# Optimization experiments

Measured on AMD Instinct MI355X. Metric: run time of the kernel, lower is better.

## Reference

```python
import jax, jax.numpy as jnp
import numpy as np

SYNCNET_T = 5
EMB_D = 512


def _l2norm(x, eps=1e-12):
    return x / jnp.maximum(jnp.linalg.norm(x, axis=-1, keepdims=True), eps)


def setup_inputs() -> dict:
    key = jax.random.key(0)
    k = jax.random.split(key, 6)
    b = 256
    a_1 = jax.random.normal(k[0], (b, 1, 80, 16), dtype=jnp.float32)
    a_2 = jax.random.normal(k[1], (b, 1, 80, 16), dtype=jnp.float32)
    v_1 = jax.random.normal(k[2], (b, 3, SYNCNET_T, 96, 96), dtype=jnp.float32)
    v_2 = jax.random.normal(k[3], (b, 3, SYNCNET_T, 96, 96), dtype=jnp.float32)
    da = 1 * 80 * 16
    dv = 3 * SYNCNET_T * 48 * 96
    W_a = jax.random.normal(k[4], (da, EMB_D), dtype=jnp.float32) / np.float32(np.sqrt(da))
    W_v = jax.random.normal(k[5], (dv, EMB_D), dtype=jnp.float32) / np.float32(np.sqrt(dv))
    return {"a_1": a_1, "v_1": v_1, "a_2": a_2, "v_2": v_2, "W_a": W_a, "W_v": W_v}


def reference(a_1, v_1, a_2, v_2, W_a, W_v):
    b = a_1.shape[0]
    audio = jnp.concatenate([a_1, a_2], axis=0)      # (2b,1,80,16)
    visual = jnp.concatenate([v_1, v_2], axis=0)     # (2b,3,T,96,96)
    visual = visual[:, :, :, visual.shape[3] // 2:]  # lower half -> (2b,3,T,48,96)
    # torch.cat([visual[:,:,i] for i in range(T)], dim=1) -> channel order (T,3)
    n2 = visual.shape[0]
    visual = jnp.moveaxis(visual, 2, 1).reshape(n2, 3 * SYNCNET_T, 48, 96)
    # syncnet (modeled): flatten -> linear -> L2 normalize, 512-d embeddings
    a = _l2norm(audio.reshape(n2, -1) @ W_a)  # (2b,d)
    v = _l2norm(visual.reshape(n2, -1) @ W_v)  # (2b,d)
    a1, a2 = a[:b], a[b:]
    v1, v2 = v[:b], v[b:]
    dot = lambda x, y: jnp.sum(x * y, axis=-1)
    # numerator: product of {a1,a2}x{v1,v2} + combos within audio and within visual
    numerator = (jnp.exp(dot(a1, v1)) + jnp.exp(dot(a1, v2))
                 + jnp.exp(dot(a2, v1)) + jnp.exp(dot(a2, v2))
                 + jnp.exp(dot(a1, a2)) + jnp.exp(dot(v1, v2)))  # (b,)
    # denominator: product of {a1,a2} with ALL visual embeddings v (2b)
    denominator = (jnp.exp(a1 @ v.T) + jnp.exp(a2 @ v.T)).sum(axis=1)  # (b,)
    loss = -jnp.mean(jnp.log(numerator / denominator))
    return loss
```

## Files before the change

kernel.cpp:

```cpp
#include <hip/hip_runtime.h>

typedef __attribute__((ext_vector_type(8))) short bf16x8;
typedef __attribute__((ext_vector_type(4))) float f32x4;

__device__ __forceinline__ unsigned int pk2(float a, float b) {
    unsigned int r;
    asm("v_cvt_pk_bf16_f32 %0, %1, %2" : "=v"(r) : "v"(a), "v"(b));
    return r;
}

__device__ __forceinline__ void gll16(void* lds, const void* g) {
    __builtin_amdgcn_global_load_lds(
        (__attribute__((address_space(1))) void*)(uintptr_t)g,
        (__attribute__((address_space(3))) void*)(uint32_t)(uintptr_t)lds,
        16, 0, 0);
}

__global__ __launch_bounds__(256) void conv_fused(
    const float* __restrict__ v_1, const float* __restrict__ v_2,
    const float* __restrict__ a_1, const float* __restrict__ a_2,
    const float* __restrict__ W_v, const float* __restrict__ W_a,
    unsigned short* __restrict__ Av, unsigned short* __restrict__ Wt,
    unsigned short* __restrict__ Aa, unsigned short* __restrict__ Wat,
    int doAv)
{
    __shared__ float T[64][65];
    const int tid = threadIdx.x;
    const int b = blockIdx.x;

    if (b < 8800) {
        const float* src; unsigned short* dst; int K, kt, nt;
        if (b < 8640) { src = W_v; dst = Wt;  K = 69120; kt = b >> 3; nt = b & 7; }
        else          { src = W_a; dst = Wat; K = 1280;  kt = (b - 8640) >> 3; nt = (b - 8640) & 7; }
        const int k0 = kt * 64, n0 = nt * 64;
        #pragma unroll
        for (int i = 0; i < 4; ++i) {
            const int kr = i * 16 + (tid >> 4);
            const int c4 = tid & 15;
            const float4 f = *(const float4*)(src + (size_t)(k0 + kr) * 512 + n0 + c4 * 4);
            T[c4 * 4 + 0][kr] = f.x; T[c4 * 4 + 1][kr] = f.y;
            T[c4 * 4 + 2][kr] = f.z; T[c4 * 4 + 3][kr] = f.w;
        }
        __syncthreads();
        #pragma unroll
        for (int j = 0; j < 2; ++j) {
            const int id = j * 256 + tid;
            const int nl = id >> 3, u = id & 7;
            float v[8];
            #pragma unroll
            for (int kk = 0; kk < 8; ++kk) v[kk] = T[nl][u * 8 + kk];
            uint4 o;
            o.x = pk2(v[0], v[1]); o.y = pk2(v[2], v[3]);
            o.z = pk2(v[4], v[5]); o.w = pk2(v[6], v[7]);
            *(uint4*)(dst + (size_t)(n0 + nl) * K + k0 + u * 8) = o;
        }
    } else if (b < 16480) {
        if (!doAv) return;
        const int bb = b - 8800;
        const int r = bb / 15, p = bb - r * 15;
        const float* srcb = (r < 256) ? (v_1 + (size_t)r * 138240)
                                      : (v_2 + (size_t)(r - 256) * 138240);
        const int c = p % 3, t9 = p / 3;
        const float* src = srcb + c * 46080 + t9 * 9216 + 4608;
        unsigned short* dst = Av + (size_t)r * 69120 + p * 4608;
        #pragma unroll
        for (int it = 0; it < 5; ++it) {
            const int u = it * 256 + tid;
            if (u < 1152) {
                const float4 f = *(const float4*)(src + u * 4);
                uint2 o; o.x = pk2(f.x, f.y); o.y = pk2(f.z, f.w);
                *(uint2*)(dst + u * 4) = o;
            }
        }
    } else {
        const int idx4 = (b - 16480) * 256 + tid;
        const int row = idx4 / 320;
        const int col4 = idx4 - row * 320;
        const float* src = (row < 256) ? (a_1 + (size_t)row * 1280)
                                       : (a_2 + (size_t)(row - 256) * 1280);
        const float4 f = *(const float4*)(src + col4 * 4);
        uint2 o; o.x = pk2(f.x, f.y); o.y = pk2(f.z, f.w);
        *(uint2*)(Aa + (size_t)idx4 * 4) = o;
    }
}

template<int AMODE>
__global__ __launch_bounds__(256, 3) void gemm_kernel(
    const unsigned short* __restrict__ Abf,
    const float* __restrict__ s1, const float* __restrict__ s2,
    const unsigned short* __restrict__ Bt,
    float* __restrict__ part, int K, int ksteps)
{
    __shared__ uint4 As[1024];
    __shared__ uint4 Bs[1024];

    const int tid = threadIdx.x;
    const int blk = blockIdx.x;
    const int nwg = gridDim.x;
    const int cpx = nwg >> 3;
    const int lin = (blk & 7) * cpx + (blk >> 3);
    const int z  = lin >> 4;
    const int mn = lin & 15;
    const int m0 = (mn >> 2) * 128;
    const int n0 = (mn & 3) * 128;
    const int k0 = z * ksteps * 64;
    part += (size_t)z * 262144;

    const int wid = tid >> 6, lane = tid & 63;
    const int l15 = lane & 15, lk = lane >> 4;
    const int wm = (wid >> 1) * 64, wn = (wid & 1) * 64;

    int ua[2][4], ub[2][4];
    #pragma unroll
    for (int kh = 0; kh < 2; ++kh) {
        #pragma unroll
        for (int mi = 0; mi < 4; ++mi) {
            const int row = wm + mi * 16 + l15;
            ua[kh][mi] = row * 8 + ((kh * 4 + lk) ^ (row & 7));
        }
        #pragma unroll
        for (int ni = 0; ni < 4; ++ni) {
            const int nn = wn + ni * 16 + l15;
            ub[kh][ni] = nn * 8 + ((kh * 4 + lk) ^ (nn & 7));
        }
    }

    const unsigned short* bsrc[4];
    const unsigned short* asrc[4];
    #pragma unroll
    for (int i = 0; i < 4; ++i) {
        const int u = i * 256 + tid;
        const int rw = u >> 3, c = u & 7;
        bsrc[i] = Bt + (size_t)(n0 + rw) * K + k0 + ((c ^ (rw & 7)) * 8);
        if (AMODE == 0)
            asrc[i] = Abf + (size_t)(m0 + rw) * K + k0 + ((c ^ (rw & 7)) * 8);
    }
    const int a_row = tid >> 1;
    const float* abase = nullptr;
    if (AMODE == 1) {
        const int grow = m0 + a_row;
        abase = (grow < 256) ? (s1 + (size_t)grow * 138240)
                             : (s2 + (size_t)(grow - 256) * 138240);
    }

    f32x4 acc[4][4];
    #pragma unroll
    for (int mi = 0; mi < 4; ++mi)
        #pragma unroll
        for (int ni = 0; ni < 4; ++ni) acc[mi][ni] = f32x4{0.f, 0.f, 0.f, 0.f};

    int kc = k0;
    for (int ks = 0; ks < ksteps; ++ks) {
        #pragma unroll
        for (int i = 0; i < 4; ++i)
            gll16(Bs + i * 256 + wid * 64, bsrc[i]);
        if (AMODE == 0) {
            #pragma unroll
            for (int i = 0; i < 4; ++i)
                gll16(As + i * 256 + wid * 64, asrc[i]);
        } else {
            #pragma unroll
            for (int x4 = 0; x4 < 4; ++x4) {
                const int x = (tid & 1) * 4 + x4;
                const int kg = kc + x * 8;
                const int p = kg / 4608;
                const int j = kg - p * 4608;
                const int c3 = p % 3, t9 = p / 3;
                const float* ap = abase + c3 * 46080 + t9 * 9216 + 4608 + j;
                const float4 f0 = *(const float4*)ap;
                const float4 f1 = *(const float4*)(ap + 4);
                uint4 pa;
                pa.x = pk2(f0.x, f0.y); pa.y = pk2(f0.z, f0.w);
                pa.z = pk2(f1.x, f1.y); pa.w = pk2(f1.z, f1.w);
                As[a_row * 8 + (x ^ (a_row & 7))] = pa;
            }
        }
        __syncthreads();

        #pragma unroll
        for (int kh = 0; kh < 2; ++kh) {
            bf16x8 af[4], bfr[4];
            #pragma unroll
            for (int mi = 0; mi < 4; ++mi) af[mi] = __builtin_bit_cast(bf16x8, As[ua[kh][mi]]);
            #pragma unroll
            for (int ni = 0; ni < 4; ++ni) bfr[ni] = __builtin_bit_cast(bf16x8, Bs[ub[kh][ni]]);
            #pragma unroll
            for (int mi = 0; mi < 4; ++mi)
                #pragma unroll
                for (int ni = 0; ni < 4; ++ni)
                    acc[mi][ni] = __builtin_amdgcn_mfma_f32_16x16x32_bf16(af[mi], bfr[ni], acc[mi][ni], 0, 0, 0);
        }
        __syncthreads();

        kc += 64;
        #pragma unroll
        for (int i = 0; i < 4; ++i) bsrc[i] += 64;
        if (AMODE == 0) {
            #pragma unroll
            for (int i = 0; i < 4; ++i) asrc[i] += 64;
        }
    }

    #pragma unroll
    for (int mi = 0; mi < 4; ++mi)
        #pragma unroll
        for (int ni = 0; ni < 4; ++ni) {
            const int col = n0 + wn + ni * 16 + l15;
            #pragma unroll
            for (int r = 0; r < 4; ++r) {
                const int row = m0 + wm + mi * 16 + lk * 4 + r;
                part[(size_t)row * 512 + col] = acc[mi][ni][r];
            }
        }
}

__global__ __launch_bounds__(256) void norm_kernel(
    const float* __restrict__ partA, const float* __restrict__ partV,
    float* __restrict__ Aout, float* __restrict__ Vout, int nzV)
{
    const int row = blockIdx.x;
    const int tid = threadIdx.x;
    const bool isV = row >= 512;
    const int r = isV ? (row - 512) : row;
    const int c0 = tid, c1 = tid + 256;

    float v0 = 0.f, v1 = 0.f;
    if (isV) {
        for (int zz = 0; zz < nzV; ++zz) {
            const float* p = partV + (size_t)zz * 262144 + (size_t)r * 512;
            v0 += p[c0]; v1 += p[c1];
        }
    } else {
        #pragma unroll
        for (int zz = 0; zz < 2; ++zz) {
            const float* p = partA + (size_t)zz * 262144 + (size_t)r * 512;
            v0 += p[c0]; v1 += p[c1];
        }
    }

    float ss = v0 * v0 + v1 * v1;
    #pragma unroll
    for (int off = 32; off > 0; off >>= 1) ss += __shfl_down(ss, off);
    __shared__ float sbuf[4];
    if ((tid & 63) == 0) sbuf[tid >> 6] = ss;
    __syncthreads();
    const float total = sbuf[0] + sbuf[1] + sbuf[2] + sbuf[3];
    const float inv = 1.f / fmaxf(sqrtf(total), 1e-12f);

    float* outp = (isV ? Vout : Aout) + (size_t)r * 512;
    outp[c0] = v0 * inv;
    outp[c1] = v1 * inv;
}

__global__ __launch_bounds__(256) void sim_kernel(
    const float* __restrict__ A, const float* __restrict__ V,
    float* __restrict__ den, float* __restrict__ num)
{
    __shared__ uint4 As[2][256];
    __shared__ uint4 Bs[2][256];

    const int tid = threadIdx.x;
    const int m0 = (blockIdx.x >> 3) * 64;
    const int n0 = (blockIdx.x & 7) * 64;
    const int nsteps = 16;

    const int a_row = tid >> 2, a_kb = tid & 3;
    const int b_col = tid & 63, b_kb = tid >> 6;
    const int a_u = (a_kb * 64 + a_row) ^ (a_kb << 1);
    const int b_u = (b_kb * 64 + b_col) ^ (b_kb << 1);

    const float* abase = A + (size_t)(m0 + a_row) * 512;
    const float* bptr  = V + (size_t)(n0 + b_col) * 512 + b_kb * 8;
    int aoff = a_kb * 8;

    const int lane = tid & 63, wid = tid >> 6;
    const int wrow = (wid >> 1) * 32, wcol = (wid & 1) * 32;
    const int l15 = lane & 15, lk = lane >> 4;

    int ra[2], rb[2];
    #pragma unroll
    for (int m = 0; m < 2; ++m) ra[m] = (lk * 64 + wrow + m * 16 + l15) ^ (lk << 1);
    #pragma unroll
    for (int n = 0; n < 2; ++n) rb[n] = (lk * 64 + wcol + n * 16 + l15) ^ (lk << 1);

    f32x4 acc[2][2];
    #pragma unroll
    for (int m = 0; m < 2; ++m)
        #pragma unroll
        for (int n = 0; n < 2; ++n) acc[m][n] = f32x4{0.f, 0.f, 0.f, 0.f};

    float4 A0 = *(const float4*)(abase + aoff);
    float4 A1 = *(const float4*)(abase + aoff + 4);
    float4 B0 = *(const float4*)bptr;
    float4 B1 = *(const float4*)(bptr + 4);

    for (int ks = 0; ks < nsteps; ++ks) {
        const int cur = ks & 1;
        const bool more = (ks + 1 < nsteps);
        float4 A0n, A1n, B0n, B1n;
        if (more) {
            aoff += 32; bptr += 32;
            A0n = *(const float4*)(abase + aoff);
            A1n = *(const float4*)(abase + aoff + 4);
            B0n = *(const float4*)bptr;
            B1n = *(const float4*)(bptr + 4);
        }
        uint4 pa;
        pa.x = pk2(A0.x, A0.y); pa.y = pk2(A0.z, A0.w);
        pa.z = pk2(A1.x, A1.y); pa.w = pk2(A1.z, A1.w);
        As[cur][a_u] = pa;
        uint4 pb;
        pb.x = pk2(B0.x, B0.y); pb.y = pk2(B0.z, B0.w);
        pb.z = pk2(B1.x, B1.y); pb.w = pk2(B1.z, B1.w);
        Bs[cur][b_u] = pb;
        __syncthreads();

        bf16x8 af[2], bfr[2];
        #pragma unroll
        for (int m = 0; m < 2; ++m) af[m] = __builtin_bit_cast(bf16x8, As[cur][ra[m]]);
        #pragma unroll
        for (int n = 0; n < 2; ++n) bfr[n] = __builtin_bit_cast(bf16x8, Bs[cur][rb[n]]);
        #pragma unroll
        for (int m = 0; m < 2; ++m)
            #pragma unroll
            for (int n = 0; n < 2; ++n)
                acc[m][n] = __builtin_amdgcn_mfma_f32_16x16x32_bf16(af[m], bfr[n], acc[m][n], 0, 0, 0);

        if (more) { A0 = A0n; A1 = A1n; B0 = B0n; B1 = B1n; }
    }

    #pragma unroll
    for (int m = 0; m < 2; ++m) {
        float rs[4] = {0.f, 0.f, 0.f, 0.f};
        #pragma unroll
        for (int n = 0; n < 2; ++n) {
            const int col = n0 + wcol + n * 16 + l15;
            #pragma unroll
            for (int r = 0; r < 4; ++r) {
                const int row = m0 + wrow + m * 16 + lk * 4 + r;
                const float e = __expf(acc[m][n][r]);
                rs[r] += e;
                if (((row - col) & 255) == 0) atomicAdd(num + (row & 255), e);
            }
        }
        #pragma unroll
        for (int r = 0; r < 4; ++r) {
            float v = rs[r];
            v += __shfl_xor(v, 1);
            v += __shfl_xor(v, 2);
            v += __shfl_xor(v, 4);
            v += __shfl_xor(v, 8);
            if (l15 == 0) {
                const int row = m0 + wrow + m * 16 + lk * 4 + r;
                atomicAdd(den + (row & 255), v);
            }
        }
    }
}

__global__ __launch_bounds__(512) void zero_kernel(float* __restrict__ p) {
    p[threadIdx.x] = 0.f;
}

__global__ __launch_bounds__(256) void dots_kernel(
    const float* __restrict__ A, const float* __restrict__ V,
    float* __restrict__ num)
{
    const int b = blockIdx.x;
    const int i = b & 255;
    const float* X = (b < 256) ? A : V;
    const float* x = X + (size_t)i * 512;
    const float* y = X + (size_t)(i + 256) * 512;
    const int tid = threadIdx.x;
    float d = x[tid] * y[tid] + x[tid + 256] * y[tid + 256];
    #pragma unroll
    for (int off = 32; off > 0; off >>= 1) d += __shfl_down(d, off);
    __shared__ float sbuf[4];
    if ((tid & 63) == 0) sbuf[tid >> 6] = d;
    __syncthreads();
    if (tid == 0) atomicAdd(num + i, __expf(sbuf[0] + sbuf[1] + sbuf[2] + sbuf[3]));
}

__global__ __launch_bounds__(256) void final_kernel(
    const float* __restrict__ den, const float* __restrict__ num,
    float* __restrict__ out)
{
    const int tid = threadIdx.x;
    float v = logf(den[tid]) - logf(num[tid]);
    #pragma unroll
    for (int off = 32; off > 0; off >>= 1) v += __shfl_down(v, off);
    __shared__ float sbuf[4];
    if ((tid & 63) == 0) sbuf[tid >> 6] = v;
    __syncthreads();
    if (tid == 0) out[0] = (sbuf[0] + sbuf[1] + sbuf[2] + sbuf[3]) * (1.f / 256.f);
}

extern "C" void kernel_launch(void* const* d_in, const int* in_sizes, int n_in,
                              void* d_out, int out_size, void* d_ws, size_t ws_size,
                              hipStream_t stream)
{
    (void)in_sizes; (void)n_in; (void)out_size;
    const float* a_1 = (const float*)d_in[0];
    const float* v_1 = (const float*)d_in[1];
    const float* a_2 = (const float*)d_in[2];
    const float* v_2 = (const float*)d_in[3];
    const float* W_a = (const float*)d_in[4];
    const float* W_v = (const float*)d_in[5];
    float* out = (float*)d_out;

    const size_t F_BASE = 512  + 2 * 262144  + 2 * 262144
                        + 2 * 327680  + 17694720 ;
    auto bytes_for = [&](int kv, bool av) {
        return (F_BASE + (size_t)kv * 262144 + (av ? 17694720u : 0u)) * 4;
    };
    int KV; bool AV;
    if      (ws_size >= bytes_for(45, true))  { KV = 45; AV = true;  }
    else if (ws_size >= bytes_for(45, false)) { KV = 45; AV = false; }
    else if (ws_size >= bytes_for(15, false)) { KV = 15; AV = false; }
    else                                      { KV = 8;  AV = false; }
    const int kstepsV = 1080 / KV;

    float* cur = (float*)d_ws;
    float* den   = cur; cur += 256;
    float* num   = cur; cur += 256;
    float* Anorm = cur; cur += 262144;
    float* Vnorm = cur; cur += 262144;
    float* partA = cur; cur += 2 * 262144;
    unsigned short* Aa  = (unsigned short*)cur; cur += 327680;
    unsigned short* Wat = (unsigned short*)cur; cur += 327680;
    float* partV = cur; cur += (size_t)KV * 262144;
    unsigned short* Wt = (unsigned short*)cur; cur += 17694720;
    unsigned short* Av = (unsigned short*)cur;

    zero_kernel<<<1, 512, 0, stream>>>(den);

    conv_fused<<<17120, 256, 0, stream>>>(v_1, v_2, a_1, a_2, W_v, W_a,
                                          Av, Wt, Aa, Wat, AV ? 1 : 0);

    if (AV)
        gemm_kernel<0><<<16 * KV, 256, 0, stream>>>(Av, nullptr, nullptr, Wt,
                                                    partV, 69120, kstepsV);
    else
        gemm_kernel<1><<<16 * KV, 256, 0, stream>>>(nullptr, v_1, v_2, Wt,
                                                    partV, 69120, kstepsV);

    gemm_kernel<0><<<32, 256, 0, stream>>>(Aa, nullptr, nullptr, Wat,
                                           partA, 1280, 10);

    norm_kernel<<<1024, 256, 0, stream>>>(partA, partV, Anorm, Vnorm, KV);
    sim_kernel<<<64, 256, 0, stream>>>(Anorm, Vnorm, den, num);
    dots_kernel<<<512, 256, 0, stream>>>(Anorm, Vnorm, num);
    final_kernel<<<1, 256, 0, stream>>>(den, num, out);
}
```

Before: 199.8 us.

## Drop bf16 activation pre-conversion; convert activations inside GEMM and simplify weight transpose

Removes the separate pass that converted the cropped visual and audio activations to bf16 in workspace. Both GEMMs now load fp32 activations directly and pack them to bf16 while staging into LDS, so activations are no longer written out and read back. The weight transpose becomes a simpler kernel: each thread reads one column with strided loads and writes contiguous bf16 runs, with no LDS tile. The workspace split-K fallback levels also change. The risk is that in-GEMM conversion adds VALU work and fp32 global load traffic to the main loop, and the strided column reads in the transpose may coalesce less well.

```diff
diff --git a/kernel.cpp b/kernel.cpp
--- a/kernel.cpp
+++ b/kernel.cpp
@@ -2,6 +2,8 @@
 
 typedef __attribute__((ext_vector_type(8))) short bf16x8;
 typedef __attribute__((ext_vector_type(4))) float f32x4;
+
+#define KSA 2
 
 __device__ __forceinline__ unsigned int pk2(float a, float b) {
     unsigned int r;
@@ -16,77 +18,35 @@
         16, 0, 0);
 }
 
-__global__ __launch_bounds__(256) void conv_fused(
-    const float* __restrict__ v_1, const float* __restrict__ v_2,
-    const float* __restrict__ a_1, const float* __restrict__ a_2,
-    const float* __restrict__ W_v, const float* __restrict__ W_a,
-    unsigned short* __restrict__ Av, unsigned short* __restrict__ Wt,
-    unsigned short* __restrict__ Aa, unsigned short* __restrict__ Wat,
-    int doAv)
-{
-    __shared__ float T[64][65];
-    const int tid = threadIdx.x;
-    const int b = blockIdx.x;
-
-    if (b < 8800) {
-        const float* src; unsigned short* dst; int K, kt, nt;
-        if (b < 8640) { src = W_v; dst = Wt;  K = 69120; kt = b >> 3; nt = b & 7; }
-        else          { src = W_a; dst = Wat; K = 1280;  kt = (b - 8640) >> 3; nt = (b - 8640) & 7; }
-        const int k0 = kt * 64, n0 = nt * 64;
-        #pragma unroll
-        for (int i = 0; i < 4; ++i) {
-            const int kr = i * 16 + (tid >> 4);
-            const int c4 = tid & 15;
-            const float4 f = *(const float4*)(src + (size_t)(k0 + kr) * 512 + n0 + c4 * 4);
-            T[c4 * 4 + 0][kr] = f.x; T[c4 * 4 + 1][kr] = f.y;
-            T[c4 * 4 + 2][kr] = f.z; T[c4 * 4 + 3][kr] = f.w;
-        }
-        __syncthreads();
-        #pragma unroll
-        for (int j = 0; j < 2; ++j) {
-            const int id = j * 256 + tid;
-            const int nl = id >> 3, u = id & 7;
-            float v[8];
-            #pragma unroll
-            for (int kk = 0; kk < 8; ++kk) v[kk] = T[nl][u * 8 + kk];
-            uint4 o;
-            o.x = pk2(v[0], v[1]); o.y = pk2(v[2], v[3]);
-            o.z = pk2(v[4], v[5]); o.w = pk2(v[6], v[7]);
-            *(uint4*)(dst + (size_t)(n0 + nl) * K + k0 + u * 8) = o;
-        }
-    } else if (b < 16480) {
-        if (!doAv) return;
-        const int bb = b - 8800;
-        const int r = bb / 15, p = bb - r * 15;
-        const float* srcb = (r < 256) ? (v_1 + (size_t)r * 138240)
-                                      : (v_2 + (size_t)(r - 256) * 138240);
-        const int c = p % 3, t9 = p / 3;
-        const float* src = srcb + c * 46080 + t9 * 9216 + 4608;
-        unsigned short* dst = Av + (size_t)r * 69120 + p * 4608;
-        #pragma unroll
-        for (int it = 0; it < 5; ++it) {
-            const int u = it * 256 + tid;
-            if (u < 1152) {
-                const float4 f = *(const float4*)(src + u * 4);
-                uint2 o; o.x = pk2(f.x, f.y); o.y = pk2(f.z, f.w);
-                *(uint2*)(dst + u * 4) = o;
-            }
-        }
-    } else {
-        const int idx4 = (b - 16480) * 256 + tid;
-        const int row = idx4 / 320;
-        const int col4 = idx4 - row * 320;
-        const float* src = (row < 256) ? (a_1 + (size_t)row * 1280)
-                                       : (a_2 + (size_t)(row - 256) * 1280);
-        const float4 f = *(const float4*)(src + col4 * 4);
-        uint2 o; o.x = pk2(f.x, f.y); o.y = pk2(f.z, f.w);
-        *(uint2*)(Aa + (size_t)idx4 * 4) = o;
-    }
-}
-
-template<int AMODE>
+__global__ __launch_bounds__(256) void wtrans(
+    const float* __restrict__ Wv, const float* __restrict__ Wa,
+    unsigned short* __restrict__ Wt, unsigned short* __restrict__ Wat)
+{
+    const int b = blockIdx.x, tid = threadIdx.x;
+    const float* src; unsigned short* dst; int K, kbase, n;
+    if (b < 1080) { src = Wv; dst = Wt;  K = 69120; kbase = (b >> 1) * 128; n = (b & 1) * 256 + tid; }
+    else { const int bb = b - 1080;
+           src = Wa; dst = Wat; K = 1280;  kbase = (bb >> 1) * 128; n = (bb & 1) * 256 + tid; }
+
+    const float* sp = src + n;
+    unsigned short* dp = dst + (size_t)n * K + kbase;
+
+    for (int kk = 0; kk < 128; kk += 16) {
+        float v[16];
+        #pragma unroll
+        for (int i = 0; i < 16; ++i) v[i] = sp[(size_t)(kbase + kk + i) * 512];
+        uint4 o0, o1;
+        o0.x = pk2(v[0], v[1]);  o0.y = pk2(v[2], v[3]);
+        o0.z = pk2(v[4], v[5]);  o0.w = pk2(v[6], v[7]);
+        o1.x = pk2(v[8], v[9]);  o1.y = pk2(v[10], v[11]);
+        o1.z = pk2(v[12], v[13]); o1.w = pk2(v[14], v[15]);
+        *(uint4*)(dp + kk) = o0;
+        *(uint4*)(dp + kk + 8) = o1;
+    }
+}
+
+template<int CROP>
 __global__ __launch_bounds__(256, 3) void gemm_kernel(
-    const unsigned short* __restrict__ Abf,
     const float* __restrict__ s1, const float* __restrict__ s2,
     const unsigned short* __restrict__ Bt,
     float* __restrict__ part, int K, int ksteps)
@@ -96,8 +56,7 @@
 
     const int tid = threadIdx.x;
     const int blk = blockIdx.x;
-    const int nwg = gridDim.x;
-    const int cpx = nwg >> 3;
+    const int cpx = gridDim.x >> 3;
     const int lin = (blk & 7) * cpx + (blk >> 3);
     const int z  = lin >> 4;
     const int mn = lin & 15;
@@ -126,22 +85,18 @@
     }
 
     const unsigned short* bsrc[4];
-    const unsigned short* asrc[4];
     #pragma unroll
     for (int i = 0; i < 4; ++i) {
         const int u = i * 256 + tid;
         const int rw = u >> 3, c = u & 7;
         bsrc[i] = Bt + (size_t)(n0 + rw) * K + k0 + ((c ^ (rw & 7)) * 8);
-        if (AMODE == 0)
-            asrc[i] = Abf + (size_t)(m0 + rw) * K + k0 + ((c ^ (rw & 7)) * 8);
-    }
+    }
+
     const int a_row = tid >> 1;
-    const float* abase = nullptr;
-    if (AMODE == 1) {
-        const int grow = m0 + a_row;
-        abase = (grow < 256) ? (s1 + (size_t)grow * 138240)
-                             : (s2 + (size_t)(grow - 256) * 138240);
-    }
+    const int grow = m0 + a_row;
+    const int ROWSTR = CROP ? 138240 : 1280;
+    const float* abase = (grow < 256) ? s1 + (size_t)grow * ROWSTR
+                                      : s2 + (size_t)(grow - 256) * ROWSTR;
 
     f32x4 acc[4][4];
     #pragma unroll
@@ -154,26 +109,26 @@
         #pragma unroll
         for (int i = 0; i < 4; ++i)
             gll16(Bs + i * 256 + wid * 64, bsrc[i]);
-        if (AMODE == 0) {
-            #pragma unroll
-            for (int i = 0; i < 4; ++i)
-                gll16(As + i * 256 + wid * 64, asrc[i]);
+
+        int aoffu;
+        if (CROP) {
+            const int p = kc / 4608;
+            const int j = kc - p * 4608;
+            const int c3 = p % 3, t9 = p / 3;
+            aoffu = c3 * 46080 + t9 * 9216 + 4608 + j;
         } else {
-            #pragma unroll
-            for (int x4 = 0; x4 < 4; ++x4) {
-                const int x = (tid & 1) * 4 + x4;
-                const int kg = kc + x * 8;
-                const int p = kg / 4608;
-                const int j = kg - p * 4608;
-                const int c3 = p % 3, t9 = p / 3;
-                const float* ap = abase + c3 * 46080 + t9 * 9216 + 4608 + j;
-                const float4 f0 = *(const float4*)ap;
-                const float4 f1 = *(const float4*)(ap + 4);
-                uint4 pa;
-                pa.x = pk2(f0.x, f0.y); pa.y = pk2(f0.z, f0.w);
-                pa.z = pk2(f1.x, f1.y); pa.w = pk2(f1.z, f1.w);
-                As[a_row * 8 + (x ^ (a_row & 7))] = pa;
-            }
+            aoffu = kc;
+        }
+        #pragma unroll
+        for (int x4 = 0; x4 < 4; ++x4) {
+            const int x = (tid & 1) * 4 + x4;
+            const float* ap = abase + aoffu + x * 8;
+            const float4 f0 = *(const float4*)ap;
+            const float4 f1 = *(const float4*)(ap + 4);
+            uint4 pa;
+            pa.x = pk2(f0.x, f0.y); pa.y = pk2(f0.z, f0.w);
+            pa.z = pk2(f1.x, f1.y); pa.w = pk2(f1.z, f1.w);
+            As[a_row * 8 + (x ^ (a_row & 7))] = pa;
         }
         __syncthreads();
 
@@ -195,10 +150,6 @@
         kc += 64;
         #pragma unroll
         for (int i = 0; i < 4; ++i) bsrc[i] += 64;
-        if (AMODE == 0) {
-            #pragma unroll
-            for (int i = 0; i < 4; ++i) asrc[i] += 64;
-        }
     }
 
     #pragma unroll
@@ -232,7 +183,7 @@
         }
     } else {
         #pragma unroll
-        for (int zz = 0; zz < 2; ++zz) {
+        for (int zz = 0; zz < KSA; ++zz) {
             const float* p = partA + (size_t)zz * 262144 + (size_t)r * 512;
             v0 += p[c0]; v1 += p[c1];
         }
@@ -408,46 +359,34 @@
     const float* W_v = (const float*)d_in[5];
     float* out = (float*)d_out;
 
-    const size_t F_BASE = 512  + 2 * 262144  + 2 * 262144
-                        + 2 * 327680  + 17694720 ;
-    auto bytes_for = [&](int kv, bool av) {
-        return (F_BASE + (size_t)kv * 262144 + (av ? 17694720u : 0u)) * 4;
+    auto need = [](int ksv) -> size_t {
+        return (size_t)4 * (512 + 262144u * (4 + ksv))
+             + (size_t)2 * (35389440u + 655360u);
     };
-    int KV; bool AV;
-    if      (ws_size >= bytes_for(45, true))  { KV = 45; AV = true;  }
-    else if (ws_size >= bytes_for(45, false)) { KV = 45; AV = false; }
-    else if (ws_size >= bytes_for(15, false)) { KV = 15; AV = false; }
-    else                                      { KV = 8;  AV = false; }
-    const int kstepsV = 1080 / KV;
-
-    float* cur = (float*)d_ws;
+    int KSV;
+    if      (ws_size >= need(45)) KSV = 45;
+    else if (ws_size >= need(27)) KSV = 27;
+    else                          KSV = 9;
+    const int kstepsV = 1080 / KSV;
+
+    float* cur   = (float*)d_ws;
     float* den   = cur; cur += 256;
     float* num   = cur; cur += 256;
     float* Anorm = cur; cur += 262144;
     float* Vnorm = cur; cur += 262144;
-    float* partA = cur; cur += 2 * 262144;
-    unsigned short* Aa  = (unsigned short*)cur; cur += 327680;
-    unsigned short* Wat = (unsigned short*)cur; cur += 327680;
-    float* partV = cur; cur += (size_t)KV * 262144;
-    unsigned short* Wt = (unsigned short*)cur; cur += 17694720;
-    unsigned short* Av = (unsigned short*)cur;
+    float* partA = cur; cur += (size_t)KSA * 262144;
+    float* partV = cur; cur += (size_t)KSV * 262144;
+    unsigned short* Wt  = (unsigned short*)cur;
+    unsigned short* Wat = Wt + 35389440u;
 
     zero_kernel<<<1, 512, 0, stream>>>(den);
 
-    conv_fused<<<17120, 256, 0, stream>>>(v_1, v_2, a_1, a_2, W_v, W_a,
-                                          Av, Wt, Aa, Wat, AV ? 1 : 0);
-
-    if (AV)
-        gemm_kernel<0><<<16 * KV, 256, 0, stream>>>(Av, nullptr, nullptr, Wt,
-                                                    partV, 69120, kstepsV);
-    else
-        gemm_kernel<1><<<16 * KV, 256, 0, stream>>>(nullptr, v_1, v_2, Wt,
-                                                    partV, 69120, kstepsV);
-
-    gemm_kernel<0><<<32, 256, 0, stream>>>(Aa, nullptr, nullptr, Wat,
-                                           partA, 1280, 10);
-
-    norm_kernel<<<1024, 256, 0, stream>>>(partA, partV, Anorm, Vnorm, KV);
+    wtrans<<<1100, 256, 0, stream>>>(W_v, W_a, Wt, Wat);
+
+    gemm_kernel<1><<<16 * KSV, 256, 0, stream>>>(v_1, v_2, Wt, partV, 69120, kstepsV);
+    gemm_kernel<0><<<16 * KSA, 256, 0, stream>>>(a_1, a_2, Wat, partA, 1280, 10);
+
+    norm_kernel<<<1024, 256, 0, stream>>>(partA, partV, Anorm, Vnorm, KSV);
     sim_kernel<<<64, 256, 0, stream>>>(Anorm, Vnorm, den, num);
     dots_kernel<<<512, 256, 0, stream>>>(Anorm, Vnorm, num);
     final_kernel<<<1, 256, 0, stream>>>(den, num, out);
```

Measured after the change: 311.1 us. 55.7% more time.
